# Kernel optimization log

Hardware: AMD Instinct MI355X
Metric: run time of the kernel (lower is better)

Reference implementation:

```python
import jax, jax.numpy as jnp
import numpy as np

N = 10000      # num nodes
E = 160000     # num edges (before self-loops)
D_IN = 512
D_HID = 512
D_OUT = 512
C = 64         # num classes


def setup_inputs() -> dict:
    key = jax.random.key(0)
    ks = jax.random.split(key, 8)
    x = jax.random.normal(ks[0], (N, D_IN), dtype=jnp.float32)
    edge_index = jax.random.randint(ks[1], (2, E), 0, N, dtype=jnp.int64)
    W1 = jax.random.normal(ks[2], (D_IN, D_HID), jnp.float32) / np.sqrt(D_IN)
    b1 = jnp.zeros((D_HID,), jnp.float32)
    W2 = jax.random.normal(ks[3], (D_HID, D_OUT), jnp.float32) / np.sqrt(D_HID)
    b2 = jnp.zeros((D_OUT,), jnp.float32)
    Wc = jax.random.normal(ks[4], (D_OUT, C), jnp.float32) / np.sqrt(D_OUT)
    bc = jnp.zeros((C,), jnp.float32)
    return {"x": x, "edge_index": edge_index, "W1": W1, "b1": b1,
            "W2": W2, "b2": b2, "Wc": Wc, "bc": bc}


def _gcn_conv(x, src, dst, ew, W, b):
    """GCNConv: symmetric degree-normalized scatter-add. ew = edge weights."""
    h = x @ W  # [N, D_out] dense GEMM
    deg = jax.ops.segment_sum(ew, dst, num_segments=N)  # in-degree incl. loops
    dis = jnp.where(deg > 0, jax.lax.rsqrt(jnp.maximum(deg, 1e-12)), 0.0)
    norm = dis[src] * dis[dst] * ew  # [E+N]
    out = jax.ops.segment_sum(h[src] * norm[:, None], dst, num_segments=N)
    return out + b


def reference(x, edge_index, W1, b1, W2, b2, Wc, bc):
    src, dst = edge_index[0], edge_index[1]
    # add_remaining_self_loops: drop existing self-loops, add one per node
    loops = jnp.arange(N, dtype=edge_index.dtype)
    src_f = jnp.concatenate([src, loops])
    dst_f = jnp.concatenate([dst, loops])
    ew = jnp.concatenate([(src != dst).astype(jnp.float32),
                          jnp.ones((N,), jnp.float32)])
    h = jax.nn.relu(_gcn_conv(x, src_f, dst_f, ew, W1, b1))
    h = _gcn_conv(h, src_f, dst_f, ew, W2, b2)
    logits = h @ Wc + bc
    return logits, jax.nn.log_softmax(logits, axis=1)
```

## Files before the change

kernel.cpp:

```cpp
#include <hip/hip_runtime.h>
#include <hip/hip_bf16.h>

#define N_NODES 10000
#define DIM 512
#define NCLS 64
#define BM 64
#define BN 128
#define BK 64
#define ELLW 64

typedef __hip_bfloat16 bf16;
typedef unsigned short u16;
typedef __attribute__((ext_vector_type(8))) short short8;
typedef __attribute__((ext_vector_type(4))) float f32x4;

__device__ __forceinline__ float b2f(bf16 v) { return __bfloat162float(v); }
__device__ __forceinline__ float ldIn(const void* p, size_t i, int isb) {
    return isb ? b2f(((const bf16*)p)[i]) : ((const float*)p)[i];
}
__device__ __forceinline__ int getE(const int* ei, int is64, int flat) {
    return is64 ? ei[2 * (size_t)flat] : ei[flat];
}
__device__ __forceinline__ void load_lds16(const bf16* g, bf16* l) {
    __builtin_amdgcn_global_load_lds(
        (const __attribute__((address_space(1))) void*)g,
        (__attribute__((address_space(3))) void*)l, 16, 0, 0);
}

__global__ void init_kernel(const u16* x16, const int* ei, int* flags, int* cursor) {
    int i = blockIdx.x * blockDim.x + threadIdx.x;
    if (i < N_NODES) cursor[i] = 0;
    if (blockIdx.x == 0 && threadIdx.x < 64) {
        int l = threadIdx.x;
        int cf = 0;
        #pragma unroll
        for (int j = 0; j < 4; j++) {
            int e = (x16[l * 4 + j] >> 7) & 0xFF;
            cf += (e >= 97 && e <= 157) ? 1 : 0;
        }
        #pragma unroll
        for (int o = 32; o > 0; o >>= 1) cf += __shfl_xor(cf, o, 64);
        int cz = (l < 32) ? ((ei[2 * l + 1] == 0) ? 1 : 0) : 0;
        #pragma unroll
        for (int o = 32; o > 0; o >>= 1) cz += __shfl_xor(cz, o, 64);
        if (l == 0) { flags[0] = (cf >= 200) ? 1 : 0; flags[1] = (cz >= 16) ? 1 : 0; }
    }
}

__global__ __launch_bounds__(256) void convert_all(
        const void* __restrict__ X, const void* __restrict__ W1,
        const void* __restrict__ W2, const void* __restrict__ Wc,
        const int* __restrict__ ei, const int* __restrict__ flags,
        int* __restrict__ cursor, int* __restrict__ ell,
        bf16* __restrict__ Xb, bf16* __restrict__ Wt1, bf16* __restrict__ Wt2,
        bf16* __restrict__ Wtc, int E) {
    __shared__ float tile[32][33];
    int b = blockIdx.x, t = threadIdx.x;
    if (b < 2500) {
        int isb = flags[0];
        int base = (b * 256 + t) * 8;
        bf16 o[8];
        if (isb) {
            *(uint4*)o = *(const uint4*)((const bf16*)X + base);
        } else {
            const float* Xf = (const float*)X + base;
            float4 v0 = *(const float4*)Xf, v1 = *(const float4*)(Xf + 4);
            o[0] = __float2bfloat16(v0.x); o[1] = __float2bfloat16(v0.y);
            o[2] = __float2bfloat16(v0.z); o[3] = __float2bfloat16(v0.w);
            o[4] = __float2bfloat16(v1.x); o[5] = __float2bfloat16(v1.y);
            o[6] = __float2bfloat16(v1.z); o[7] = __float2bfloat16(v1.w);
        }
        *(uint4*)&Xb[base] = *(uint4*)o;
    } else if (b < 3044) {
        int isb = flags[0];
        const void* W; bf16* Wt; int N; int bb;
        if (b < 2756)      { W = W1; Wt = Wt1; N = DIM;  bb = b - 2500; }
        else if (b < 3012) { W = W2; Wt = Wt2; N = DIM;  bb = b - 2756; }
        else               { W = Wc; Wt = Wtc; N = NCLS; bb = b - 3012; }
        int nt = N / 32;
        int n0 = (bb % nt) * 32, k0 = (bb / nt) * 32;
        int tx = t & 31, ty = t >> 5;
        for (int r = ty; r < 32; r += 8)
            tile[r][tx] = ldIn(W, (size_t)(k0 + r) * N + n0 + tx, isb);
        __syncthreads();
        for (int r = ty; r < 32; r += 8)
            Wt[(size_t)(n0 + r) * DIM + k0 + tx] = __float2bfloat16(tile[tx][r]);
    } else {
        int e = (b - 3044) * 256 + t;
        if (e >= E) return;
        int is64 = flags[1];
        int s = getE(ei, is64, e), d = getE(ei, is64, E + e);
        if (s == d || (unsigned)s >= N_NODES || (unsigned)d >= N_NODES) return;
        int pos = atomicAdd(&cursor[d], 1);
        ell[d * ELLW + (pos & (ELLW - 1))] = s;
    }
}

__global__ __launch_bounds__(256) void gemm_mfma(
        const bf16* __restrict__ A, const bf16* __restrict__ Bt,
        bf16* __restrict__ C, int M, int Nc, int K,
        const int* __restrict__ deg) {
    __shared__ bf16 At[BM * BK];
    __shared__ bf16 Bts[BN * BK];
    int t = threadIdx.x;
    int w = t >> 6, l = t & 63;
    int bm = blockIdx.y * BM, bn = blockIdx.x * BN;
    int wn = w * 32;

    f32x4 acc[4][2] = {};
    int srow8 = l >> 3;
    int sk8b  = (l & 7) * 8;

    for (int k0 = 0; k0 < K; k0 += BK) {
        __syncthreads();
        #pragma unroll
        for (int i = 0; i < 2; i++) {
            int c = w * 2 + i;
            load_lds16(A + (size_t)(bm + c * 8 + srow8) * K + k0 + sk8b, &At[c * 512]);
        }
        #pragma unroll
        for (int i = 0; i < 4; i++) {
            int c = w * 4 + i;
            load_lds16(Bt + (size_t)(bn + c * 8 + srow8) * K + k0 + sk8b, &Bts[c * 512]);
        }
        __syncthreads();

        #pragma unroll
        for (int kk = 0; kk < BK; kk += 32) {
            short8 af[4], bf[2];
            #pragma unroll
            for (int i = 0; i < 4; i++)
                af[i] = *(const short8*)&At[(i * 16 + (l & 15)) * BK + kk + (l >> 4) * 8];
            #pragma unroll
            for (int j = 0; j < 2; j++)
                bf[j] = *(const short8*)&Bts[(wn + j * 16 + (l & 15)) * BK + kk + (l >> 4) * 8];
            #pragma unroll
            for (int i = 0; i < 4; i++)
                #pragma unroll
                for (int j = 0; j < 2; j++)
                    acc[i][j] = __builtin_amdgcn_mfma_f32_16x16x32_bf16(
                                    af[i], bf[j], acc[i][j], 0, 0, 0);
        }
    }

    int col = l & 15, rq = (l >> 4) * 4;
    #pragma unroll
    for (int i = 0; i < 4; i++) {
        #pragma unroll
        for (int r = 0; r < 4; r++) {
            int gm = bm + i * 16 + rq + r;
            if (gm >= M) continue;
            float rs = rsqrtf((float)deg[gm] + 1.0f);
            #pragma unroll
            for (int j = 0; j < 2; j++) {
                int gn = bn + wn + j * 16 + col;
                C[(size_t)gm * Nc + gn] = __float2bfloat16(acc[i][j][r] * rs);
            }
        }
    }
}

__global__ __launch_bounds__(256) void gather_ell(
        const int* __restrict__ cursor, const int* __restrict__ ell,
        const bf16* __restrict__ Hs, const void* __restrict__ bias,
        const int* __restrict__ flags, bf16* __restrict__ Out, int relu) {
    int wid = (int)((blockIdx.x * (size_t)blockDim.x + threadIdx.x) >> 6);
    int lane = threadIdx.x & 63;
    if (wid >= N_NODES) return;
    int cnt0 = cursor[wid];
    int cnt = min(cnt0, ELLW);
    int idx = ell[wid * ELLW + lane];

    float acc[8];
    bf16 v[8];
    *(uint4*)v = *(const uint4*)(Hs + (size_t)wid * DIM + lane * 8);
    #pragma unroll
    for (int j = 0; j < 8; j++) acc[j] = b2f(v[j]);

    int e = 0;
    for (; e + 7 < cnt; e += 8) {
        bf16 r[8][8];
        #pragma unroll
        for (int b = 0; b < 8; b++) {
            int s = __shfl(idx, e + b, 64);
            *(uint4*)r[b] = *(const uint4*)(Hs + (size_t)s * DIM + lane * 8);
        }
        #pragma unroll
        for (int j = 0; j < 8; j++)
            acc[j] += ((b2f(r[0][j]) + b2f(r[1][j])) + (b2f(r[2][j]) + b2f(r[3][j])))
                    + ((b2f(r[4][j]) + b2f(r[5][j])) + (b2f(r[6][j]) + b2f(r[7][j])));
    }
    for (; e < cnt; e++) {
        int s = __shfl(idx, e, 64);
        *(uint4*)v = *(const uint4*)(Hs + (size_t)s * DIM + lane * 8);
        #pragma unroll
        for (int j = 0; j < 8; j++) acc[j] += b2f(v[j]);
    }

    float ds = rsqrtf((float)cnt0 + 1.0f);
    int ibias = flags[0];
    bf16 o[8];
    #pragma unroll
    for (int j = 0; j < 8; j++) {
        float val = acc[j] * ds + ldIn(bias, lane * 8 + j, ibias);
        if (relu) val = fmaxf(val, 0.0f);
        o[j] = __float2bfloat16(val);
    }
    *(uint4*)(Out + (size_t)wid * DIM + lane * 8) = *(uint4*)o;
}

__global__ __launch_bounds__(64) void cls_lsm_kernel(
        const bf16* __restrict__ A, const bf16* __restrict__ Wct,
        const void* __restrict__ bias, const int* __restrict__ flags,
        float* __restrict__ out, int M) {
    int l = threadIdx.x;
    int row0 = blockIdx.x * 16;
    int q = l >> 4, col15 = l & 15;

    f32x4 acc[4] = {};
    #pragma unroll 4
    for (int k0 = 0; k0 < DIM; k0 += 32) {
        short8 af = *(const short8*)&A[(size_t)(row0 + col15) * DIM + k0 + q * 8];
        #pragma unroll
        for (int j = 0; j < 4; j++) {
            short8 bf = *(const short8*)&Wct[(size_t)(j * 16 + col15) * DIM + k0 + q * 8];
            acc[j] = __builtin_amdgcn_mfma_f32_16x16x32_bf16(af, bf, acc[j], 0, 0, 0);
        }
    }

    int ibias = flags[0];
    float bcol[4];
    #pragma unroll
    for (int j = 0; j < 4; j++) bcol[j] = ldIn(bias, j * 16 + col15, ibias);

    #pragma unroll
    for (int r = 0; r < 4; r++) {
        int row = row0 + q * 4 + r;
        float v[4];
        #pragma unroll
        for (int j = 0; j < 4; j++) v[j] = acc[j][r] + bcol[j];
        float m = fmaxf(fmaxf(v[0], v[1]), fmaxf(v[2], v[3]));
        #pragma unroll
        for (int o = 8; o > 0; o >>= 1) m = fmaxf(m, __shfl_xor(m, o, 64));
        float s = __expf(v[0] - m) + __expf(v[1] - m) + __expf(v[2] - m) + __expf(v[3] - m);
        #pragma unroll
        for (int o = 8; o > 0; o >>= 1) s += __shfl_xor(s, o, 64);
        float lse = m + __logf(s);
        if (row < M) {
            #pragma unroll
            for (int j = 0; j < 4; j++) {
                out[(size_t)row * NCLS + j * 16 + col15] = v[j];
                out[(size_t)M * NCLS + (size_t)row * NCLS + j * 16 + col15] = v[j] - lse;
            }
        }
    }
}

extern "C" void kernel_launch(void* const* d_in, const int* in_sizes, int n_in,
                              void* d_out, int out_size, void* d_ws, size_t ws_size,
                              hipStream_t stream) {
    const void* x  = d_in[0];
    const int*  ei = (const int*)d_in[1];
    const void* W1 = d_in[2];
    const void* b1 = d_in[3];
    const void* W2 = d_in[4];
    const void* b2 = d_in[5];
    const void* Wc = d_in[6];
    const void* bc = d_in[7];
    float* out = (float*)d_out;
    int E = in_sizes[1] / 2;

    char* ws = (char*)d_ws;
    int*   flags  = (int*)ws;
    int*   cursor = (int*)(ws + 65536);
    int*   ell    = (int*)(ws + 131072);
    bf16*  xb     = (bf16*) (ws + 4194304);
    bf16*  Wt1    = (bf16*) (ws + 14680064);
    bf16*  Wt2    = (bf16*) (ws + 15204352);
    bf16*  Wct    = (bf16*) (ws + 15728640);
    bf16*  B0     = (bf16*) (ws + 16777216);
    bf16*  B1     = (bf16*) (ws + 27262976);

    int gN = (N_NODES * 64 + 255) / 256;
    dim3 gg(DIM / BN, (N_NODES + BM - 1) / BM);
    int gConv = 3044 + (E + 255) / 256;

    init_kernel<<<(N_NODES + 255) / 256, 256, 0, stream>>>((const u16*)x, ei, flags, cursor);
    convert_all<<<gConv, 256, 0, stream>>>(x, W1, W2, Wc, ei, flags, cursor, ell,
                                           xb, Wt1, Wt2, Wct, E);

    gemm_mfma<<<gg, 256, 0, stream>>>(xb, Wt1, B0, N_NODES, DIM, DIM, cursor);
    gather_ell<<<gN, 256, 0, stream>>>(cursor, ell, B0, b1, flags, B1, 1);

    gemm_mfma<<<gg, 256, 0, stream>>>(B1, Wt2, B0, N_NODES, DIM, DIM, cursor);
    gather_ell<<<gN, 256, 0, stream>>>(cursor, ell, B0, b2, flags, B1, 0);

    cls_lsm_kernel<<<(N_NODES + 15) / 16, 64, 0, stream>>>(B1, Wct, bc, flags, out, N_NODES);
}
```

Before: 192.3 us.

## Fuse all GCN stages into one persistent cooperative kernel with grid syncs

Replaces the seven separate launches (init, convert, two GEMMs, two gathers, classifier) with a single persistent cooperative kernel. The phases are separated by grid-wide barriers, and the GEMM tiles, gather rows and classifier groups are distributed with grid-stride loops. It also XOR-swizzles the GEMM LDS layout to reduce bank conflicts. The goal is to remove launch overhead and inter-kernel gaps, at the cost of capping the grid at the occupancy limit (at most 1024 blocks) and paying for several grid.sync barriers, with lower parallelism per phase.

```diff
diff --git a/kernel.cpp b/kernel.cpp
--- a/kernel.cpp
+++ b/kernel.cpp
@@ -1,5 +1,8 @@
 #include <hip/hip_runtime.h>
 #include <hip/hip_bf16.h>
+#include <hip/hip_cooperative_groups.h>
+
+namespace cg = cooperative_groups;
 
 #define N_NODES 10000
 #define DIM 512
@@ -8,6 +11,9 @@
 #define BN 128
 #define BK 64
 #define ELLW 64
+#define NTILES ((DIM / BN) * ((N_NODES + BM - 1) / BM))
+#define XCONV_BLKS 2500
+#define TRANS_BLKS 544
 
 typedef __hip_bfloat16 bf16;
 typedef unsigned short u16;
@@ -27,11 +33,183 @@
         (__attribute__((address_space(3))) void*)l, 16, 0, 0);
 }
 
-__global__ void init_kernel(const u16* x16, const int* ei, int* flags, int* cursor) {
-    int i = blockIdx.x * blockDim.x + threadIdx.x;
-    if (i < N_NODES) cursor[i] = 0;
-    if (blockIdx.x == 0 && threadIdx.x < 64) {
-        int l = threadIdx.x;
+struct Args {
+    const void *X, *W1, *b1, *W2, *b2, *Wc, *bc;
+    const int* ei;
+    int *cursor, *ell;
+    bf16 *Xb, *Wt1, *Wt2, *Wtc, *B0, *B1;
+    float* out;
+    int E;
+};
+
+__device__ void gemm_phase(const bf16* __restrict__ A, const bf16* __restrict__ Bt,
+                           bf16* __restrict__ C, const int* __restrict__ deg,
+                           char* smraw, int bid, int nb, int t) {
+    bf16* At  = (bf16*)smraw;
+    bf16* Bts = (bf16*)(smraw + BM * BK * 2);
+    int w = t >> 6, l = t & 63;
+    int srow8 = l >> 3;
+    int sk8b  = (((l & 7) ^ srow8) * 8);
+
+    for (int tile = bid; tile < NTILES; tile += nb) {
+        int bm = (tile >> 2) * BM, bn = (tile & 3) * BN;
+        f32x4 acc[4][2] = {};
+
+        for (int k0 = 0; k0 < DIM; k0 += BK) {
+            __syncthreads();
+            #pragma unroll
+            for (int i = 0; i < 2; i++) {
+                int c = w * 2 + i;
+                load_lds16(A + (size_t)(bm + c * 8 + srow8) * DIM + k0 + sk8b, &At[c * 512]);
+            }
+            #pragma unroll
+            for (int i = 0; i < 4; i++) {
+                int c = w * 4 + i;
+                load_lds16(Bt + (size_t)(bn + c * 8 + srow8) * DIM + k0 + sk8b, &Bts[c * 512]);
+            }
+            __syncthreads();
+
+            #pragma unroll
+            for (int kk = 0; kk < BK; kk += 32) {
+                short8 af[4], bfr[2];
+                int slot = (((kk >> 3) + (l >> 4)) ^ (l & 7)) * 8;
+                #pragma unroll
+                for (int i = 0; i < 4; i++)
+                    af[i] = *(const short8*)&At[(i * 16 + (l & 15)) * BK + slot];
+                #pragma unroll
+                for (int j = 0; j < 2; j++)
+                    bfr[j] = *(const short8*)&Bts[(w * 32 + j * 16 + (l & 15)) * BK + slot];
+                #pragma unroll
+                for (int i = 0; i < 4; i++)
+                    #pragma unroll
+                    for (int j = 0; j < 2; j++)
+                        acc[i][j] = __builtin_amdgcn_mfma_f32_16x16x32_bf16(
+                                        af[i], bfr[j], acc[i][j], 0, 0, 0);
+            }
+        }
+
+        int col = l & 15, rq = (l >> 4) * 4;
+        #pragma unroll
+        for (int i = 0; i < 4; i++) {
+            #pragma unroll
+            for (int r = 0; r < 4; r++) {
+                int gm = bm + i * 16 + rq + r;
+                if (gm >= N_NODES) continue;
+                float rs = rsqrtf((float)deg[gm] + 1.0f);
+                #pragma unroll
+                for (int j = 0; j < 2; j++) {
+                    int gn = bn + w * 32 + j * 16 + col;
+                    C[(size_t)gm * DIM + gn] = __float2bfloat16(acc[i][j][r] * rs);
+                }
+            }
+        }
+    }
+}
+
+__device__ void gather_phase(const int* __restrict__ cursor, const int* __restrict__ ell,
+                             const bf16* __restrict__ Hs, const void* __restrict__ bias,
+                             int isb, bf16* __restrict__ Out, int relu,
+                             int bid, int nb, int w, int lane) {
+    for (int wid = bid * 4 + w; wid < N_NODES; wid += nb * 4) {
+        int cnt0 = cursor[wid];
+        int cnt = min(cnt0, ELLW);
+        int idx = ell[wid * ELLW + lane];
+
+        float acc[8];
+        bf16 v[8];
+        *(uint4*)v = *(const uint4*)(Hs + (size_t)wid * DIM + lane * 8);
+        #pragma unroll
+        for (int j = 0; j < 8; j++) acc[j] = b2f(v[j]);
+
+        int e = 0;
+        for (; e + 7 < cnt; e += 8) {
+            bf16 r[8][8];
+            #pragma unroll
+            for (int b = 0; b < 8; b++) {
+                int s = __shfl(idx, e + b, 64);
+                *(uint4*)r[b] = *(const uint4*)(Hs + (size_t)s * DIM + lane * 8);
+            }
+            #pragma unroll
+            for (int j = 0; j < 8; j++)
+                acc[j] += ((b2f(r[0][j]) + b2f(r[1][j])) + (b2f(r[2][j]) + b2f(r[3][j])))
+                        + ((b2f(r[4][j]) + b2f(r[5][j])) + (b2f(r[6][j]) + b2f(r[7][j])));
+        }
+        for (; e < cnt; e++) {
+            int s = __shfl(idx, e, 64);
+            *(uint4*)v = *(const uint4*)(Hs + (size_t)s * DIM + lane * 8);
+            #pragma unroll
+            for (int j = 0; j < 8; j++) acc[j] += b2f(v[j]);
+        }
+
+        float ds = rsqrtf((float)cnt0 + 1.0f);
+        bf16 o[8];
+        #pragma unroll
+        for (int j = 0; j < 8; j++) {
+            float val = acc[j] * ds + ldIn(bias, lane * 8 + j, isb);
+            if (relu) val = fmaxf(val, 0.0f);
+            o[j] = __float2bfloat16(val);
+        }
+        *(uint4*)(Out + (size_t)wid * DIM + lane * 8) = *(uint4*)o;
+    }
+}
+
+__device__ void cls_phase(const bf16* __restrict__ A, const bf16* __restrict__ Wct,
+                          const void* __restrict__ bias, int isb, float* __restrict__ out,
+                          int bid, int nb, int w, int l) {
+    const int NG = (N_NODES + 15) / 16;
+    for (int g = bid * 4 + w; g < NG; g += nb * 4) {
+        int row0 = g * 16;
+        int q = l >> 4, col15 = l & 15;
+
+        f32x4 acc[4] = {};
+        #pragma unroll 4
+        for (int k0 = 0; k0 < DIM; k0 += 32) {
+            short8 af = *(const short8*)&A[(size_t)(row0 + col15) * DIM + k0 + q * 8];
+            #pragma unroll
+            for (int j = 0; j < 4; j++) {
+                short8 bfr = *(const short8*)&Wct[(size_t)(j * 16 + col15) * DIM + k0 + q * 8];
+                acc[j] = __builtin_amdgcn_mfma_f32_16x16x32_bf16(af, bfr, acc[j], 0, 0, 0);
+            }
+        }
+
+        float bcol[4];
+        #pragma unroll
+        for (int j = 0; j < 4; j++) bcol[j] = ldIn(bias, j * 16 + col15, isb);
+
+        #pragma unroll
+        for (int r = 0; r < 4; r++) {
+            int row = row0 + q * 4 + r;
+            float v[4];
+            #pragma unroll
+            for (int j = 0; j < 4; j++) v[j] = acc[j][r] + bcol[j];
+            float m = fmaxf(fmaxf(v[0], v[1]), fmaxf(v[2], v[3]));
+            #pragma unroll
+            for (int o = 8; o > 0; o >>= 1) m = fmaxf(m, __shfl_xor(m, o, 64));
+            float s = __expf(v[0] - m) + __expf(v[1] - m) + __expf(v[2] - m) + __expf(v[3] - m);
+            #pragma unroll
+            for (int o = 8; o > 0; o >>= 1) s += __shfl_xor(s, o, 64);
+            float lse = m + __logf(s);
+            if (row < N_NODES) {
+                #pragma unroll
+                for (int j = 0; j < 4; j++) {
+                    out[(size_t)row * NCLS + j * 16 + col15] = v[j];
+                    out[(size_t)N_NODES * NCLS + (size_t)row * NCLS + j * 16 + col15] = v[j] - lse;
+                }
+            }
+        }
+    }
+}
+
+__global__ __launch_bounds__(256) void mega(Args a) {
+    cg::grid_group grid = cg::this_grid();
+    __shared__ __align__(16) char smraw[(BM + BN) * BK * 2];
+    __shared__ int sflags[2];
+
+    int t = threadIdx.x, bid = blockIdx.x, nb = gridDim.x;
+    int w = t >> 6, l = t & 63;
+
+    if (t < 64) {
+        const u16* x16 = (const u16*)a.X;
         int cf = 0;
         #pragma unroll
         for (int j = 0; j < 4; j++) {
@@ -40,260 +218,103 @@
         }
         #pragma unroll
         for (int o = 32; o > 0; o >>= 1) cf += __shfl_xor(cf, o, 64);
-        int cz = (l < 32) ? ((ei[2 * l + 1] == 0) ? 1 : 0) : 0;
+        int cz = (l < 32) ? ((a.ei[2 * l + 1] == 0) ? 1 : 0) : 0;
         #pragma unroll
         for (int o = 32; o > 0; o >>= 1) cz += __shfl_xor(cz, o, 64);
-        if (l == 0) { flags[0] = (cf >= 200) ? 1 : 0; flags[1] = (cz >= 16) ? 1 : 0; }
-    }
-}
-
-__global__ __launch_bounds__(256) void convert_all(
-        const void* __restrict__ X, const void* __restrict__ W1,
-        const void* __restrict__ W2, const void* __restrict__ Wc,
-        const int* __restrict__ ei, const int* __restrict__ flags,
-        int* __restrict__ cursor, int* __restrict__ ell,
-        bf16* __restrict__ Xb, bf16* __restrict__ Wt1, bf16* __restrict__ Wt2,
-        bf16* __restrict__ Wtc, int E) {
-    __shared__ float tile[32][33];
-    int b = blockIdx.x, t = threadIdx.x;
-    if (b < 2500) {
-        int isb = flags[0];
-        int base = (b * 256 + t) * 8;
-        bf16 o[8];
-        if (isb) {
-            *(uint4*)o = *(const uint4*)((const bf16*)X + base);
+        if (l == 0) { sflags[0] = (cf >= 200) ? 1 : 0; sflags[1] = (cz >= 16) ? 1 : 0; }
+    }
+    __syncthreads();
+    int isb = sflags[0], is64 = sflags[1];
+
+    int nell = (a.E + 255) >> 8;
+    for (int u = bid; u < XCONV_BLKS + TRANS_BLKS + nell; u += nb) {
+        if (u < XCONV_BLKS) {
+            int base = (u * 256 + t) * 8;
+            bf16 o[8];
+            if (isb) {
+                *(uint4*)o = *(const uint4*)((const bf16*)a.X + base);
+            } else {
+                const float* Xf = (const float*)a.X + base;
+                float4 v0 = *(const float4*)Xf, v1 = *(const float4*)(Xf + 4);
+                o[0] = __float2bfloat16(v0.x); o[1] = __float2bfloat16(v0.y);
+                o[2] = __float2bfloat16(v0.z); o[3] = __float2bfloat16(v0.w);
+                o[4] = __float2bfloat16(v1.x); o[5] = __float2bfloat16(v1.y);
+                o[6] = __float2bfloat16(v1.z); o[7] = __float2bfloat16(v1.w);
+            }
+            *(uint4*)&a.Xb[base] = *(uint4*)o;
+        } else if (u < XCONV_BLKS + TRANS_BLKS) {
+            float (*tile)[33] = (float(*)[33])smraw;
+            int bb = u - XCONV_BLKS;
+            const void* W; bf16* Wt; int N;
+            if (bb < 256)      { W = a.W1; Wt = a.Wt1; N = DIM; }
+            else if (bb < 512) { W = a.W2; Wt = a.Wt2; N = DIM;  bb -= 256; }
+            else               { W = a.Wc; Wt = a.Wtc; N = NCLS; bb -= 512; }
+            int nt = N / 32;
+            int n0 = (bb % nt) * 32, k0 = (bb / nt) * 32;
+            int tx = t & 31, ty = t >> 5;
+            __syncthreads();
+            for (int r = ty; r < 32; r += 8)
+                tile[r][tx] = ldIn(W, (size_t)(k0 + r) * N + n0 + tx, isb);
+            __syncthreads();
+            for (int r = ty; r < 32; r += 8)
+                Wt[(size_t)(n0 + r) * DIM + k0 + tx] = __float2bfloat16(tile[tx][r]);
         } else {
-            const float* Xf = (const float*)X + base;
-            float4 v0 = *(const float4*)Xf, v1 = *(const float4*)(Xf + 4);
-            o[0] = __float2bfloat16(v0.x); o[1] = __float2bfloat16(v0.y);
-            o[2] = __float2bfloat16(v0.z); o[3] = __float2bfloat16(v0.w);
-            o[4] = __float2bfloat16(v1.x); o[5] = __float2bfloat16(v1.y);
-            o[6] = __float2bfloat16(v1.z); o[7] = __float2bfloat16(v1.w);
-        }
-        *(uint4*)&Xb[base] = *(uint4*)o;
-    } else if (b < 3044) {
-        int isb = flags[0];
-        const void* W; bf16* Wt; int N; int bb;
-        if (b < 2756)      { W = W1; Wt = Wt1; N = DIM;  bb = b - 2500; }
-        else if (b < 3012) { W = W2; Wt = Wt2; N = DIM;  bb = b - 2756; }
-        else               { W = Wc; Wt = Wtc; N = NCLS; bb = b - 3012; }
-        int nt = N / 32;
-        int n0 = (bb % nt) * 32, k0 = (bb / nt) * 32;
-        int tx = t & 31, ty = t >> 5;
-        for (int r = ty; r < 32; r += 8)
-            tile[r][tx] = ldIn(W, (size_t)(k0 + r) * N + n0 + tx, isb);
-        __syncthreads();
-        for (int r = ty; r < 32; r += 8)
-            Wt[(size_t)(n0 + r) * DIM + k0 + tx] = __float2bfloat16(tile[tx][r]);
-    } else {
-        int e = (b - 3044) * 256 + t;
-        if (e >= E) return;
-        int is64 = flags[1];
-        int s = getE(ei, is64, e), d = getE(ei, is64, E + e);
-        if (s == d || (unsigned)s >= N_NODES || (unsigned)d >= N_NODES) return;
-        int pos = atomicAdd(&cursor[d], 1);
-        ell[d * ELLW + (pos & (ELLW - 1))] = s;
-    }
-}
-
-__global__ __launch_bounds__(256) void gemm_mfma(
-        const bf16* __restrict__ A, const bf16* __restrict__ Bt,
-        bf16* __restrict__ C, int M, int Nc, int K,
-        const int* __restrict__ deg) {
-    __shared__ bf16 At[BM * BK];
-    __shared__ bf16 Bts[BN * BK];
-    int t = threadIdx.x;
-    int w = t >> 6, l = t & 63;
-    int bm = blockIdx.y * BM, bn = blockIdx.x * BN;
-    int wn = w * 32;
-
-    f32x4 acc[4][2] = {};
-    int srow8 = l >> 3;
-    int sk8b  = (l & 7) * 8;
-
-    for (int k0 = 0; k0 < K; k0 += BK) {
-        __syncthreads();
-        #pragma unroll
-        for (int i = 0; i < 2; i++) {
-            int c = w * 2 + i;
-            load_lds16(A + (size_t)(bm + c * 8 + srow8) * K + k0 + sk8b, &At[c * 512]);
-        }
-        #pragma unroll
-        for (int i = 0; i < 4; i++) {
-            int c = w * 4 + i;
-            load_lds16(Bt + (size_t)(bn + c * 8 + srow8) * K + k0 + sk8b, &Bts[c * 512]);
-        }
-        __syncthreads();
-
-        #pragma unroll
-        for (int kk = 0; kk < BK; kk += 32) {
-            short8 af[4], bf[2];
-            #pragma unroll
-            for (int i = 0; i < 4; i++)
-                af[i] = *(const short8*)&At[(i * 16 + (l & 15)) * BK + kk + (l >> 4) * 8];
-            #pragma unroll
-            for (int j = 0; j < 2; j++)
-                bf[j] = *(const short8*)&Bts[(wn + j * 16 + (l & 15)) * BK + kk + (l >> 4) * 8];
-            #pragma unroll
-            for (int i = 0; i < 4; i++)
-                #pragma unroll
-                for (int j = 0; j < 2; j++)
-                    acc[i][j] = __builtin_amdgcn_mfma_f32_16x16x32_bf16(
-                                    af[i], bf[j], acc[i][j], 0, 0, 0);
-        }
-    }
-
-    int col = l & 15, rq = (l >> 4) * 4;
-    #pragma unroll
-    for (int i = 0; i < 4; i++) {
-        #pragma unroll
-        for (int r = 0; r < 4; r++) {
-            int gm = bm + i * 16 + rq + r;
-            if (gm >= M) continue;
-            float rs = rsqrtf((float)deg[gm] + 1.0f);
-            #pragma unroll
-            for (int j = 0; j < 2; j++) {
-                int gn = bn + wn + j * 16 + col;
-                C[(size_t)gm * Nc + gn] = __float2bfloat16(acc[i][j][r] * rs);
-            }
-        }
-    }
-}
-
-__global__ __launch_bounds__(256) void gather_ell(
-        const int* __restrict__ cursor, const int* __restrict__ ell,
-        const bf16* __restrict__ Hs, const void* __restrict__ bias,
-        const int* __restrict__ flags, bf16* __restrict__ Out, int relu) {
-    int wid = (int)((blockIdx.x * (size_t)blockDim.x + threadIdx.x) >> 6);
-    int lane = threadIdx.x & 63;
-    if (wid >= N_NODES) return;
-    int cnt0 = cursor[wid];
-    int cnt = min(cnt0, ELLW);
-    int idx = ell[wid * ELLW + lane];
-
-    float acc[8];
-    bf16 v[8];
-    *(uint4*)v = *(const uint4*)(Hs + (size_t)wid * DIM + lane * 8);
-    #pragma unroll
-    for (int j = 0; j < 8; j++) acc[j] = b2f(v[j]);
-
-    int e = 0;
-    for (; e + 7 < cnt; e += 8) {
-        bf16 r[8][8];
-        #pragma unroll
-        for (int b = 0; b < 8; b++) {
-            int s = __shfl(idx, e + b, 64);
-            *(uint4*)r[b] = *(const uint4*)(Hs + (size_t)s * DIM + lane * 8);
-        }
-        #pragma unroll
-        for (int j = 0; j < 8; j++)
-            acc[j] += ((b2f(r[0][j]) + b2f(r[1][j])) + (b2f(r[2][j]) + b2f(r[3][j])))
-                    + ((b2f(r[4][j]) + b2f(r[5][j])) + (b2f(r[6][j]) + b2f(r[7][j])));
-    }
-    for (; e < cnt; e++) {
-        int s = __shfl(idx, e, 64);
-        *(uint4*)v = *(const uint4*)(Hs + (size_t)s * DIM + lane * 8);
-        #pragma unroll
-        for (int j = 0; j < 8; j++) acc[j] += b2f(v[j]);
-    }
-
-    float ds = rsqrtf((float)cnt0 + 1.0f);
-    int ibias = flags[0];
-    bf16 o[8];
-    #pragma unroll
-    for (int j = 0; j < 8; j++) {
-        float val = acc[j] * ds + ldIn(bias, lane * 8 + j, ibias);
-        if (relu) val = fmaxf(val, 0.0f);
-        o[j] = __float2bfloat16(val);
-    }
-    *(uint4*)(Out + (size_t)wid * DIM + lane * 8) = *(uint4*)o;
-}
-
-__global__ __launch_bounds__(64) void cls_lsm_kernel(
-        const bf16* __restrict__ A, const bf16* __restrict__ Wct,
-        const void* __restrict__ bias, const int* __restrict__ flags,
-        float* __restrict__ out, int M) {
-    int l = threadIdx.x;
-    int row0 = blockIdx.x * 16;
-    int q = l >> 4, col15 = l & 15;
-
-    f32x4 acc[4] = {};
-    #pragma unroll 4
-    for (int k0 = 0; k0 < DIM; k0 += 32) {
-        short8 af = *(const short8*)&A[(size_t)(row0 + col15) * DIM + k0 + q * 8];
-        #pragma unroll
-        for (int j = 0; j < 4; j++) {
-            short8 bf = *(const short8*)&Wct[(size_t)(j * 16 + col15) * DIM + k0 + q * 8];
-            acc[j] = __builtin_amdgcn_mfma_f32_16x16x32_bf16(af, bf, acc[j], 0, 0, 0);
-        }
-    }
-
-    int ibias = flags[0];
-    float bcol[4];
-    #pragma unroll
-    for (int j = 0; j < 4; j++) bcol[j] = ldIn(bias, j * 16 + col15, ibias);
-
-    #pragma unroll
-    for (int r = 0; r < 4; r++) {
-        int row = row0 + q * 4 + r;
-        float v[4];
-        #pragma unroll
-        for (int j = 0; j < 4; j++) v[j] = acc[j][r] + bcol[j];
-        float m = fmaxf(fmaxf(v[0], v[1]), fmaxf(v[2], v[3]));
-        #pragma unroll
-        for (int o = 8; o > 0; o >>= 1) m = fmaxf(m, __shfl_xor(m, o, 64));
-        float s = __expf(v[0] - m) + __expf(v[1] - m) + __expf(v[2] - m) + __expf(v[3] - m);
-        #pragma unroll
-        for (int o = 8; o > 0; o >>= 1) s += __shfl_xor(s, o, 64);
-        float lse = m + __logf(s);
-        if (row < M) {
-            #pragma unroll
-            for (int j = 0; j < 4; j++) {
-                out[(size_t)row * NCLS + j * 16 + col15] = v[j];
-                out[(size_t)M * NCLS + (size_t)row * NCLS + j * 16 + col15] = v[j] - lse;
-            }
-        }
-    }
+            int e = (u - XCONV_BLKS - TRANS_BLKS) * 256 + t;
+            if (e < a.E) {
+                int s = getE(a.ei, is64, e), d = getE(a.ei, is64, a.E + e);
+                if (!(s == d || (unsigned)s >= N_NODES || (unsigned)d >= N_NODES)) {
+                    int pos = atomicAdd(&a.cursor[d], 1);
+                    a.ell[d * ELLW + (pos & (ELLW - 1))] = s;
+                }
+            }
+        }
+    }
+
+    __threadfence();  grid.sync();
+    gemm_phase(a.Xb, a.Wt1, a.B0, a.cursor, smraw, bid, nb, t);
+    __threadfence();  grid.sync();
+    gather_phase(a.cursor, a.ell, a.B0, a.b1, isb, a.B1, 1, bid, nb, w, l);
+    __threadfence();  grid.sync();
+    gemm_phase(a.B1, a.Wt2, a.B0, a.cursor, smraw, bid, nb, t);
+    __threadfence();  grid.sync();
+    gather_phase(a.cursor, a.ell, a.B0, a.b2, isb, a.B1, 0, bid, nb, w, l);
+    __threadfence();  grid.sync();
+    cls_phase(a.B1, a.Wtc, a.bc, isb, a.out, bid, nb, w, l);
 }
 
 extern "C" void kernel_launch(void* const* d_in, const int* in_sizes, int n_in,
                               void* d_out, int out_size, void* d_ws, size_t ws_size,
                               hipStream_t stream) {
-    const void* x  = d_in[0];
-    const int*  ei = (const int*)d_in[1];
-    const void* W1 = d_in[2];
-    const void* b1 = d_in[3];
-    const void* W2 = d_in[4];
-    const void* b2 = d_in[5];
-    const void* Wc = d_in[6];
-    const void* bc = d_in[7];
-    float* out = (float*)d_out;
-    int E = in_sizes[1] / 2;
-
     char* ws = (char*)d_ws;
-    int*   flags  = (int*)ws;
-    int*   cursor = (int*)(ws + 65536);
-    int*   ell    = (int*)(ws + 131072);
-    bf16*  xb     = (bf16*) (ws + 4194304);
-    bf16*  Wt1    = (bf16*) (ws + 14680064);
-    bf16*  Wt2    = (bf16*) (ws + 15204352);
-    bf16*  Wct    = (bf16*) (ws + 15728640);
-    bf16*  B0     = (bf16*) (ws + 16777216);
-    bf16*  B1     = (bf16*) (ws + 27262976);
-
-    int gN = (N_NODES * 64 + 255) / 256;
-    dim3 gg(DIM / BN, (N_NODES + BM - 1) / BM);
-    int gConv = 3044 + (E + 255) / 256;
-
-    init_kernel<<<(N_NODES + 255) / 256, 256, 0, stream>>>((const u16*)x, ei, flags, cursor);
-    convert_all<<<gConv, 256, 0, stream>>>(x, W1, W2, Wc, ei, flags, cursor, ell,
-                                           xb, Wt1, Wt2, Wct, E);
-
-    gemm_mfma<<<gg, 256, 0, stream>>>(xb, Wt1, B0, N_NODES, DIM, DIM, cursor);
-    gather_ell<<<gN, 256, 0, stream>>>(cursor, ell, B0, b1, flags, B1, 1);
-
-    gemm_mfma<<<gg, 256, 0, stream>>>(B1, Wt2, B0, N_NODES, DIM, DIM, cursor);
-    gather_ell<<<gN, 256, 0, stream>>>(cursor, ell, B0, b2, flags, B1, 0);
-
-    cls_lsm_kernel<<<(N_NODES + 15) / 16, 64, 0, stream>>>(B1, Wct, bc, flags, out, N_NODES);
-}
+    Args a;
+    a.X  = d_in[0];
+    a.ei = (const int*)d_in[1];
+    a.W1 = d_in[2]; a.b1 = d_in[3];
+    a.W2 = d_in[4]; a.b2 = d_in[5];
+    a.Wc = d_in[6]; a.bc = d_in[7];
+    a.out = (float*)d_out;
+    a.E = in_sizes[1] / 2;
+
+    a.cursor = (int*) (ws + 65536);
+    a.ell    = (int*) (ws + 131072);
+    a.Xb     = (bf16*)(ws + 4194304);
+    a.Wt1    = (bf16*)(ws + 14680064);
+    a.Wt2    = (bf16*)(ws + 15204352);
+    a.Wtc    = (bf16*)(ws + 15728640);
+    a.B0     = (bf16*)(ws + 16777216);
+    a.B1     = (bf16*)(ws + 27262976);
+
+    hipMemsetAsync(a.cursor, 0, N_NODES * sizeof(int), stream);
+
+    static int maxb = 0;
+    if (maxb == 0) {
+        if (hipOccupancyMaxActiveBlocksPerMultiprocessor(&maxb, mega, 256, 0) != hipSuccess
+            || maxb < 1)
+            maxb = 2;
+    }
+    int grid = maxb * 256;
+    if (grid > 1024) grid = 1024;
+
+    void* args[] = { (void*)&a };
+    hipLaunchCooperativeKernel(mega, dim3(grid), dim3(256), args, 0, stream);
+}
```

After: 540.1 us. 2.81x slower.

## Split gather across column chunks, fold dtype detection into convert, pre-convert biases

Applied to the files above, without the earlier changes.

The gather kernel now uses one wave per (node, 128-column chunk) rather than one wave per node. That gives four times as many waves, each issuing 4-byte loads instead of 16-byte loads, to raise parallelism for the irregular neighbour reads. The init kernel is replaced by a memset, and every convert_all block recomputes the dtype flags locally. One extra block converts the biases to fp32 once so the gather and classifier skip the dtype branch. Narrower loads can reduce memory efficiency per request, and the ELL index load is repeated in every chunk.

```diff
diff --git a/kernel.cpp b/kernel.cpp
--- a/kernel.cpp
+++ b/kernel.cpp
@@ -11,6 +11,7 @@
 
 typedef __hip_bfloat16 bf16;
 typedef unsigned short u16;
+typedef unsigned int u32;
 typedef __attribute__((ext_vector_type(8))) short short8;
 typedef __attribute__((ext_vector_type(4))) float f32x4;
 
@@ -26,38 +27,42 @@
         (const __attribute__((address_space(1))) void*)g,
         (__attribute__((address_space(3))) void*)l, 16, 0, 0);
 }
-
-__global__ void init_kernel(const u16* x16, const int* ei, int* flags, int* cursor) {
-    int i = blockIdx.x * blockDim.x + threadIdx.x;
-    if (i < N_NODES) cursor[i] = 0;
-    if (blockIdx.x == 0 && threadIdx.x < 64) {
-        int l = threadIdx.x;
-        int cf = 0;
-        #pragma unroll
-        for (int j = 0; j < 4; j++) {
-            int e = (x16[l * 4 + j] >> 7) & 0xFF;
-            cf += (e >= 97 && e <= 157) ? 1 : 0;
-        }
-        #pragma unroll
-        for (int o = 32; o > 0; o >>= 1) cf += __shfl_xor(cf, o, 64);
-        int cz = (l < 32) ? ((ei[2 * l + 1] == 0) ? 1 : 0) : 0;
-        #pragma unroll
-        for (int o = 32; o > 0; o >>= 1) cz += __shfl_xor(cz, o, 64);
-        if (l == 0) { flags[0] = (cf >= 200) ? 1 : 0; flags[1] = (cz >= 16) ? 1 : 0; }
-    }
-}
+__device__ __forceinline__ float blo(u32 v) { union {u32 u; float f;} x; x.u = v << 16; return x.f; }
+__device__ __forceinline__ float bhi(u32 v) { union {u32 u; float f;} x; x.u = v & 0xffff0000u; return x.f; }
+__device__ __forceinline__ u16  f2b(float f) { bf16 h = __float2bfloat16(f); return *(u16*)&h; }
 
 __global__ __launch_bounds__(256) void convert_all(
         const void* __restrict__ X, const void* __restrict__ W1,
         const void* __restrict__ W2, const void* __restrict__ Wc,
-        const int* __restrict__ ei, const int* __restrict__ flags,
+        const void* __restrict__ b1, const void* __restrict__ b2,
+        const void* __restrict__ bc, const int* __restrict__ ei,
         int* __restrict__ cursor, int* __restrict__ ell,
         bf16* __restrict__ Xb, bf16* __restrict__ Wt1, bf16* __restrict__ Wt2,
-        bf16* __restrict__ Wtc, int E) {
+        bf16* __restrict__ Wtc, float* __restrict__ bF1, float* __restrict__ bF2,
+        float* __restrict__ bFc, int E) {
     __shared__ float tile[32][33];
+    __shared__ int sflags[2];
     int b = blockIdx.x, t = threadIdx.x;
+
+    if (t < 64) {
+        const u16* x16 = (const u16*)X;
+        int cf = 0;
+        #pragma unroll
+        for (int j = 0; j < 4; j++) {
+            int e = (x16[t * 4 + j] >> 7) & 0xFF;
+            cf += (e >= 97 && e <= 157) ? 1 : 0;
+        }
+        #pragma unroll
+        for (int o = 32; o > 0; o >>= 1) cf += __shfl_xor(cf, o, 64);
+        int cz = (t < 32) ? ((ei[2 * t + 1] == 0) ? 1 : 0) : 0;
+        #pragma unroll
+        for (int o = 32; o > 0; o >>= 1) cz += __shfl_xor(cz, o, 64);
+        if (t == 0) { sflags[0] = (cf >= 200) ? 1 : 0; sflags[1] = (cz >= 16) ? 1 : 0; }
+    }
+    __syncthreads();
+    int isb = sflags[0], is64 = sflags[1];
+
     if (b < 2500) {
-        int isb = flags[0];
         int base = (b * 256 + t) * 8;
         bf16 o[8];
         if (isb) {
@@ -72,11 +77,10 @@
         }
         *(uint4*)&Xb[base] = *(uint4*)o;
     } else if (b < 3044) {
-        int isb = flags[0];
-        const void* W; bf16* Wt; int N; int bb;
-        if (b < 2756)      { W = W1; Wt = Wt1; N = DIM;  bb = b - 2500; }
-        else if (b < 3012) { W = W2; Wt = Wt2; N = DIM;  bb = b - 2756; }
-        else               { W = Wc; Wt = Wtc; N = NCLS; bb = b - 3012; }
+        const void* W; bf16* Wt; int N; int bb = b - 2500;
+        if (bb < 256)      { W = W1; Wt = Wt1; N = DIM; }
+        else if (bb < 512) { W = W2; Wt = Wt2; N = DIM;  bb -= 256; }
+        else               { W = Wc; Wt = Wtc; N = NCLS; bb -= 512; }
         int nt = N / 32;
         int n0 = (bb % nt) * 32, k0 = (bb / nt) * 32;
         int tx = t & 31, ty = t >> 5;
@@ -85,10 +89,15 @@
         __syncthreads();
         for (int r = ty; r < 32; r += 8)
             Wt[(size_t)(n0 + r) * DIM + k0 + tx] = __float2bfloat16(tile[tx][r]);
+    } else if (b == 3044) {
+        for (int i = t; i < 2 * DIM + NCLS; i += 256) {
+            if (i < DIM)            bF1[i] = ldIn(b1, i, isb);
+            else if (i < 2 * DIM)   bF2[i - DIM] = ldIn(b2, i - DIM, isb);
+            else                    bFc[i - 2 * DIM] = ldIn(bc, i - 2 * DIM, isb);
+        }
     } else {
-        int e = (b - 3044) * 256 + t;
+        int e = (b - 3045) * 256 + t;
         if (e >= E) return;
-        int is64 = flags[1];
         int s = getE(ei, is64, e), d = getE(ei, is64, E + e);
         if (s == d || (unsigned)s >= N_NODES || (unsigned)d >= N_NODES) return;
         int pos = atomicAdd(&cursor[d], 1);
@@ -127,19 +136,19 @@
 
         #pragma unroll
         for (int kk = 0; kk < BK; kk += 32) {
-            short8 af[4], bf[2];
+            short8 af[4], bfr[2];
             #pragma unroll
             for (int i = 0; i < 4; i++)
                 af[i] = *(const short8*)&At[(i * 16 + (l & 15)) * BK + kk + (l >> 4) * 8];
             #pragma unroll
             for (int j = 0; j < 2; j++)
-                bf[j] = *(const short8*)&Bts[(wn + j * 16 + (l & 15)) * BK + kk + (l >> 4) * 8];
+                bfr[j] = *(const short8*)&Bts[(wn + j * 16 + (l & 15)) * BK + kk + (l >> 4) * 8];
             #pragma unroll
             for (int i = 0; i < 4; i++)
                 #pragma unroll
                 for (int j = 0; j < 2; j++)
                     acc[i][j] = __builtin_amdgcn_mfma_f32_16x16x32_bf16(
-                                    af[i], bf[j], acc[i][j], 0, 0, 0);
+                                    af[i], bfr[j], acc[i][j], 0, 0, 0);
         }
     }
 
@@ -162,57 +171,51 @@
 
 __global__ __launch_bounds__(256) void gather_ell(
         const int* __restrict__ cursor, const int* __restrict__ ell,
-        const bf16* __restrict__ Hs, const void* __restrict__ bias,
-        const int* __restrict__ flags, bf16* __restrict__ Out, int relu) {
-    int wid = (int)((blockIdx.x * (size_t)blockDim.x + threadIdx.x) >> 6);
-    int lane = threadIdx.x & 63;
+        const bf16* __restrict__ Hs, const float* __restrict__ bias,
+        bf16* __restrict__ Out, int relu) {
+    int t = threadIdx.x;
+    int w = t >> 6, lane = t & 63;
+    int chunk = blockIdx.x & 3;
+    int wid = (blockIdx.x >> 2) * 4 + w;
     if (wid >= N_NODES) return;
+    int c0 = chunk * 128 + lane * 2;
     int cnt0 = cursor[wid];
     int cnt = min(cnt0, ELLW);
     int idx = ell[wid * ELLW + lane];
 
-    float acc[8];
-    bf16 v[8];
-    *(uint4*)v = *(const uint4*)(Hs + (size_t)wid * DIM + lane * 8);
-    #pragma unroll
-    for (int j = 0; j < 8; j++) acc[j] = b2f(v[j]);
+    u32 v = *(const u32*)(Hs + (size_t)wid * DIM + c0);
+    float a0 = blo(v), a1 = bhi(v);
 
     int e = 0;
     for (; e + 7 < cnt; e += 8) {
-        bf16 r[8][8];
+        u32 r[8];
         #pragma unroll
         for (int b = 0; b < 8; b++) {
             int s = __shfl(idx, e + b, 64);
-            *(uint4*)r[b] = *(const uint4*)(Hs + (size_t)s * DIM + lane * 8);
-        }
-        #pragma unroll
-        for (int j = 0; j < 8; j++)
-            acc[j] += ((b2f(r[0][j]) + b2f(r[1][j])) + (b2f(r[2][j]) + b2f(r[3][j])))
-                    + ((b2f(r[4][j]) + b2f(r[5][j])) + (b2f(r[6][j]) + b2f(r[7][j])));
+            r[b] = *(const u32*)(Hs + (size_t)s * DIM + c0);
+        }
+        a0 += ((blo(r[0]) + blo(r[1])) + (blo(r[2]) + blo(r[3])))
+            + ((blo(r[4]) + blo(r[5])) + (blo(r[6]) + blo(r[7])));
+        a1 += ((bhi(r[0]) + bhi(r[1])) + (bhi(r[2]) + bhi(r[3])))
+            + ((bhi(r[4]) + bhi(r[5])) + (bhi(r[6]) + bhi(r[7])));
     }
     for (; e < cnt; e++) {
         int s = __shfl(idx, e, 64);
-        *(uint4*)v = *(const uint4*)(Hs + (size_t)s * DIM + lane * 8);
-        #pragma unroll
-        for (int j = 0; j < 8; j++) acc[j] += b2f(v[j]);
+        u32 rv = *(const u32*)(Hs + (size_t)s * DIM + c0);
+        a0 += blo(rv); a1 += bhi(rv);
     }
 
     float ds = rsqrtf((float)cnt0 + 1.0f);
-    int ibias = flags[0];
-    bf16 o[8];
-    #pragma unroll
-    for (int j = 0; j < 8; j++) {
-        float val = acc[j] * ds + ldIn(bias, lane * 8 + j, ibias);
-        if (relu) val = fmaxf(val, 0.0f);
-        o[j] = __float2bfloat16(val);
-    }
-    *(uint4*)(Out + (size_t)wid * DIM + lane * 8) = *(uint4*)o;
+    float v0 = a0 * ds + bias[c0];
+    float v1 = a1 * ds + bias[c0 + 1];
+    if (relu) { v0 = fmaxf(v0, 0.0f); v1 = fmaxf(v1, 0.0f); }
+    u32 o = (u32)f2b(v0) | ((u32)f2b(v1) << 16);
+    *(u32*)(Out + (size_t)wid * DIM + c0) = o;
 }
 
 __global__ __launch_bounds__(64) void cls_lsm_kernel(
         const bf16* __restrict__ A, const bf16* __restrict__ Wct,
-        const void* __restrict__ bias, const int* __restrict__ flags,
-        float* __restrict__ out, int M) {
+        const float* __restrict__ bias, float* __restrict__ out, int M) {
     int l = threadIdx.x;
     int row0 = blockIdx.x * 16;
     int q = l >> 4, col15 = l & 15;
@@ -223,15 +226,14 @@
         short8 af = *(const short8*)&A[(size_t)(row0 + col15) * DIM + k0 + q * 8];
         #pragma unroll
         for (int j = 0; j < 4; j++) {
-            short8 bf = *(const short8*)&Wct[(size_t)(j * 16 + col15) * DIM + k0 + q * 8];
-            acc[j] = __builtin_amdgcn_mfma_f32_16x16x32_bf16(af, bf, acc[j], 0, 0, 0);
-        }
-    }
-
-    int ibias = flags[0];
+            short8 bfr = *(const short8*)&Wct[(size_t)(j * 16 + col15) * DIM + k0 + q * 8];
+            acc[j] = __builtin_amdgcn_mfma_f32_16x16x32_bf16(af, bfr, acc[j], 0, 0, 0);
+        }
+    }
+
     float bcol[4];
     #pragma unroll
-    for (int j = 0; j < 4; j++) bcol[j] = ldIn(bias, j * 16 + col15, ibias);
+    for (int j = 0; j < 4; j++) bcol[j] = bias[j * 16 + col15];
 
     #pragma unroll
     for (int r = 0; r < 4; r++) {
@@ -271,7 +273,9 @@
     int E = in_sizes[1] / 2;
 
     char* ws = (char*)d_ws;
-    int*   flags  = (int*)ws;
+    float* bF1    = (float*)ws;
+    float* bF2    = (float*)(ws + 4096);
+    float* bFc    = (float*)(ws + 8192);
     int*   cursor = (int*)(ws + 65536);
     int*   ell    = (int*)(ws + 131072);
     bf16*  xb     = (bf16*) (ws + 4194304);
@@ -281,19 +285,19 @@
     bf16*  B0     = (bf16*) (ws + 16777216);
     bf16*  B1     = (bf16*) (ws + 27262976);
 
-    int gN = (N_NODES * 64 + 255) / 256;
     dim3 gg(DIM / BN, (N_NODES + BM - 1) / BM);
-    int gConv = 3044 + (E + 255) / 256;
-
-    init_kernel<<<(N_NODES + 255) / 256, 256, 0, stream>>>((const u16*)x, ei, flags, cursor);
-    convert_all<<<gConv, 256, 0, stream>>>(x, W1, W2, Wc, ei, flags, cursor, ell,
-                                           xb, Wt1, Wt2, Wct, E);
+    int gConv = 3045 + (E + 255) / 256;
+
+    hipMemsetAsync(cursor, 0, N_NODES * sizeof(int), stream);
+    convert_all<<<gConv, 256, 0, stream>>>(x, W1, W2, Wc, b1, b2, bc, ei,
+                                           cursor, ell, xb, Wt1, Wt2, Wct,
+                                           bF1, bF2, bFc, E);
 
     gemm_mfma<<<gg, 256, 0, stream>>>(xb, Wt1, B0, N_NODES, DIM, DIM, cursor);
-    gather_ell<<<gN, 256, 0, stream>>>(cursor, ell, B0, b1, flags, B1, 1);
+    gather_ell<<<N_NODES, 256, 0, stream>>>(cursor, ell, B0, bF1, B1, 1);
 
     gemm_mfma<<<gg, 256, 0, stream>>>(B1, Wt2, B0, N_NODES, DIM, DIM, cursor);
-    gather_ell<<<gN, 256, 0, stream>>>(cursor, ell, B0, b2, flags, B1, 0);
-
-    cls_lsm_kernel<<<(N_NODES + 15) / 16, 64, 0, stream>>>(B1, Wct, bc, flags, out, N_NODES);
-}
+    gather_ell<<<N_NODES, 256, 0, stream>>>(cursor, ell, B0, bF2, B1, 0);
+
+    cls_lsm_kernel<<<(N_NODES + 15) / 16, 64, 0, stream>>>(B1, Wct, bFc, out, N_NODES);
+}
```

Result: faster. 180.1 us (-6.3%).
